# Performance work log

Measured on AMD Instinct MI355X. Metric: run time of the kernel, lower is better.

Reference implementation:

```python
import jax, jax.numpy as jnp
import numpy as np

B, N, NP, K, C_IN, C, H = 16, 4096, 1024, 32, 128, 256, 4
C_G = C_IN + 3  # grouped feature dim (use_xyz concat of relative coords)
EPS = 1e-3      # keras LayerNormalization default epsilon


def setup_inputs() -> dict:
    key = jax.random.key(0)
    ks = jax.random.split(key, 16)
    s = 0.05
    return {
        "xyz": jax.random.normal(ks[0], (B, N, 3), jnp.float32),
        "newxyz": jax.random.normal(ks[1], (B, NP, 3), jnp.float32),
        "feature_input": jax.random.normal(ks[2], (B, N, C_IN), jnp.float32),
        "w_qkv": jax.random.normal(ks[3], (C_G, 3 * C), jnp.float32) * s,
        "proj_w": jax.random.normal(ks[4], (C, C), jnp.float32) * s,
        "proj_b": jnp.zeros((C,), jnp.float32),
        "dense_w": jax.random.normal(ks[5], (C_G, C), jnp.float32) * s,
        "dense_b": jnp.zeros((C,), jnp.float32),
        "fc1_w": jax.random.normal(ks[6], (C, 2 * C), jnp.float32) * s,
        "fc1_b": jnp.zeros((2 * C,), jnp.float32),
        "fc2_w": jax.random.normal(ks[7], (2 * C, C), jnp.float32) * s,
        "fc2_b": jnp.zeros((C,), jnp.float32),
        "n1_g": jnp.ones((C_G,), jnp.float32),
        "n1_b": jnp.zeros((C_G,), jnp.float32),
        "n2_g": jnp.ones((C,), jnp.float32),
        "n2_b": jnp.zeros((C,), jnp.float32),
        "group_num": K,
        "training": True,
    }


def _layernorm(x, g, b):
    m = jnp.mean(x, axis=-1, keepdims=True)
    v = jnp.mean(jnp.square(x - m), axis=-1, keepdims=True)
    return (x - m) * jax.lax.rsqrt(v + EPS) * g + b


def _sample_and_group(newxyz, group_num, xyz, feats):
    # squared pairwise distances (B, NP, N)
    d2 = (jnp.sum(newxyz**2, -1)[:, :, None]
          - 2.0 * jnp.einsum('bpc,bnc->bpn', newxyz, xyz)
          + jnp.sum(xyz**2, -1)[:, None, :])
    _, idx = jax.lax.top_k(-d2, group_num)            # (B, NP, K) nearest
    b_idx = jnp.arange(newxyz.shape[0])[:, None, None]
    grouped_xyz = xyz[b_idx, idx] - newxyz[:, :, None, :]   # (B, NP, K, 3)
    grouped_feat = feats[b_idx, idx]                        # (B, NP, K, C_IN)
    return jnp.concatenate([grouped_xyz, grouped_feat], axis=-1)


def _self_attention(x, w_qkv, proj_w, proj_b):
    b, n, k = x.shape[0], x.shape[1], x.shape[2]
    d = C // H
    qkv = jnp.einsum('bnkc,cd->bnkd', x, w_qkv)
    qkv = qkv.reshape(b, n, k, 3, H, d)
    qkv = jnp.transpose(qkv, (3, 0, 1, 4, 2, 5))      # (3, B, NP, H, K, d)
    q, kk, v = qkv[0], qkv[1], qkv[2]
    qm = jnp.max(q, axis=-2, keepdims=True)           # (B, NP, H, 1, d)
    attn = jnp.einsum('bnhqd,bnhkd->bnhqk', qm, kk) * (C ** -0.5)
    attn = jax.nn.softmax(attn, axis=-1)
    out = jnp.einsum('bnhqk,bnhkd->bnhqd', attn, v)[..., 0, :]  # (B, NP, H, d)
    out = out.reshape(b, n, C)
    return jax.nn.relu(out @ proj_w + proj_b)


def reference(xyz, newxyz, feature_input, w_qkv, proj_w, proj_b, dense_w,
              dense_b, fc1_w, fc1_b, fc2_w, fc2_b, n1_g, n1_b, n2_g, n2_b,
              group_num, training):
    gf = _sample_and_group(newxyz, group_num, xyz, feature_input)  # (B,NP,K,C_G)
    feat = _self_attention(_layernorm(gf, n1_g, n1_b), w_qkv, proj_w, proj_b)
    feat = feat + jax.nn.relu(jnp.max(gf, axis=-2) @ dense_w + dense_b)
    f2 = _layernorm(feat, n2_g, n2_b)
    f2 = jax.nn.relu(f2 @ fc1_w + fc1_b)
    f2 = f2 @ fc2_w + fc2_b
    return f2 + feat
```

## Files before the change

kernel.cpp:

```cpp
#include <hip/hip_runtime.h>
#include <hip/hip_bf16.h>

typedef __hip_bfloat16 bf16;

#define Bn   16
#define Nn   4096
#define NPn  1024
#define Kn   32
#define CINn 128
#define CGn  131
#define Cn   256
#define Hn   4
#define KPAD 160
#define XBS  168
#define XFS2 136
#define GFS  136

typedef __attribute__((ext_vector_type(8))) short frag_ab;
typedef __attribute__((ext_vector_type(4))) float frag_cd;

__device__ __forceinline__ float b2f(bf16 x) { return __bfloat162float(x); }
__device__ __forceinline__ bf16  f2b(float x) { return __float2bfloat16(x); }
__device__ __forceinline__ short f2bs(float x) {
  union { bf16 h; short s; } u; u.h = __float2bfloat16(x); return u.s;
}
__device__ __forceinline__ float bs2f(short s) {
  union { short v; bf16 h; } u; u.v = s; return __bfloat162float(u.h);
}
__device__ __forceinline__ unsigned f2ord(float f) {
  unsigned u = __float_as_uint(f);
  return u ^ ((u >> 31) ? 0xffffffffu : 0x80000000u);
}

__global__ __launch_bounds__(256) void xyzw_prep_kernel(
    const float* __restrict__ xyz, float4* __restrict__ xyzw) {
  const int i = blockIdx.x * 256 + threadIdx.x;
  const float x = xyz[i*3 + 0];
  const float y = xyz[i*3 + 1];
  const float z = xyz[i*3 + 2];
  const float sx = __fadd_rn(__fadd_rn(__fmul_rn(x,x), __fmul_rn(y,y)),
                             __fmul_rn(z,z));
  xyzw[i] = make_float4(x, y, z, sx);
}

__global__ __launch_bounds__(256) void knn_kernel(const float4* __restrict__ xyzw,
                                                  const float* __restrict__ newxyz,
                                                  int* __restrict__ idx_out) {
  constexpr int CAP = 2048;
  __shared__ unsigned long long tmin[256];
  __shared__ __align__(16) unsigned long long cand[CAP + 4];
  __shared__ unsigned long long wtau[4];
  __shared__ unsigned long long wred[4];
  __shared__ int scnt;
  const int bp  = blockIdx.x;
  const int b   = bp >> 10;
  const int tid = threadIdx.x;
  const float qx = newxyz[bp*3 + 0];
  const float qy = newxyz[bp*3 + 1];
  const float qz = newxyz[bp*3 + 2];
  const float sn = __fadd_rn(__fadd_rn(__fmul_rn(qx,qx), __fmul_rn(qy,qy)),
                             __fmul_rn(qz,qz));
  const float4* xb = xyzw + (size_t)b * Nn;
  unsigned long long key[16];
  unsigned long long lmin = ~0ull;
  #pragma unroll
  for (int s = 0; s < 16; ++s) {
    const int n = s*256 + tid;
    const float4 xw = xb[n];
    const float dot = __fadd_rn(__fadd_rn(__fmul_rn(qx,xw.x), __fmul_rn(qy,xw.y)),
                                __fmul_rn(qz,xw.z));
    const float d2 = __fadd_rn(__fsub_rn(sn, __fmul_rn(2.0f, dot)), xw.w);
    key[s] = ((unsigned long long)f2ord(d2) << 32) | (unsigned)n;
    if (key[s] < lmin) lmin = key[s];
  }
  const int lane = tid & 63, wv = tid >> 6;

  if (tid == 0) scnt = 0;
  tmin[tid] = lmin;
  __syncthreads();

  {
    const unsigned long long* wt = &tmin[wv * 64];
    int rk = 0;
    #pragma unroll 8
    for (int j = 0; j < 64; ++j) rk += (wt[j] < lmin) ? 1 : 0;
    if (rk == 15) wtau[wv] = lmin;
  }
  __syncthreads();
  unsigned long long tau = wtau[0];
  if (wtau[1] < tau) tau = wtau[1];
  if (wtau[2] < tau) tau = wtau[2];
  if (wtau[3] < tau) tau = wtau[3];

  #pragma unroll
  for (int s = 0; s < 16; ++s) {
    if (key[s] <= tau) {
      const int p = atomicAdd(&scnt, 1);
      if (p < CAP) cand[p] = key[s];
    }
  }
  __syncthreads();
  const int m = scnt;

  if (m >= Kn && m <= CAP) {
    if (tid < 4) cand[m + tid] = ~0ull;
    __syncthreads();
    const int m4 = (m + 3) & ~3;
    for (int t = tid; t < m; t += 256) {
      const unsigned long long mykey = cand[t];
      int r = 0;
      for (int j = 0; j < m4; j += 4) {
        r += (cand[j+0] < mykey) ? 1 : 0;
        r += (cand[j+1] < mykey) ? 1 : 0;
        r += (cand[j+2] < mykey) ? 1 : 0;
        r += (cand[j+3] < mykey) ? 1 : 0;
      }
      if (r < Kn) idx_out[(size_t)bp*Kn + r] = (int)(mykey & 0xffffffffu);
    }
  } else {
    for (int s = 0; s < Kn; ++s) {
      unsigned long long mm = lmin;
      #pragma unroll
      for (int d = 32; d; d >>= 1) {
        const unsigned lo = __shfl_xor((unsigned)(mm & 0xffffffffu), d, 64);
        const unsigned hi = __shfl_xor((unsigned)(mm >> 32), d, 64);
        const unsigned long long o = ((unsigned long long)hi << 32) | lo;
        if (o < mm) mm = o;
      }
      if (lane == 0) wred[wv] = mm;
      __syncthreads();
      unsigned long long best = wred[0];
      if (wred[1] < best) best = wred[1];
      if (wred[2] < best) best = wred[2];
      if (wred[3] < best) best = wred[3];
      __syncthreads();
      const int n = (int)(best & 0xffffffffu);
      if (tid == 0) idx_out[(size_t)bp*Kn + s] = n;
      if ((n & 255) == tid) {
        const int slot = n >> 8;
        #pragma unroll
        for (int t = 0; t < 16; ++t) if (t == slot) key[t] = ~0ull;
        unsigned long long m2 = ~0ull;
        #pragma unroll
        for (int t = 0; t < 16; ++t) if (key[t] < m2) m2 = key[t];
        lmin = m2;
      }
    }
  }
}

__global__ __launch_bounds__(256) void wprep_all_kernel(
    const float* __restrict__ w_qkv, const float* __restrict__ proj_w,
    const float* __restrict__ dense_w, const float* __restrict__ fc1_w,
    const float* __restrict__ fc2_w, short* __restrict__ o_qkv,
    short* __restrict__ o_proj, short* __restrict__ o_dense,
    short* __restrict__ o_fc1, short* __restrict__ o_fc2) {
  const int blk = blockIdx.x;
  const float* W; short* out; int K, N, nnt, remap, base;
  if      (blk <  480) { W=w_qkv;   out=o_qkv;   K=CGn; N=768; nnt=48; remap=1; base=0;    }
  else if (blk <  736) { W=proj_w;  out=o_proj;  K=Cn;  N=256; nnt=16; remap=0; base=480;  }
  else if (blk <  896) { W=dense_w; out=o_dense; K=CGn; N=256; nnt=16; remap=1; base=736;  }
  else if (blk < 1408) { W=fc1_w;   out=o_fc1;   K=Cn;  N=512; nnt=32; remap=0; base=896;  }
  else                 { W=fc2_w;   out=o_fc2;   K=512; N=256; nnt=16; remap=0; base=1408; }
  const int t = (blk - base) * 256 + threadIdx.x;
  const int j    = t & 7;
  const int lane = (t >> 3) & 63;
  const int nt   = (t >> 9) % nnt;
  const int kt   = (t >> 9) / nnt;
  const int k = kt*32 + (lane >> 4)*8 + j;
  const int n = nt*16 + (lane & 15);
  int krow = k;
  if (remap) krow = (k < 128) ? k + 3 : k - 128;
  out[t] = (k < K) ? f2bs(W[(size_t)krow*N + n]) : (short)0;
}

__global__ __launch_bounds__(256, 3) void fused_attn_kernel(
    const float* __restrict__ xyz, const float* __restrict__ newxyz,
    const float* __restrict__ featin, const short* __restrict__ wfrag,
    const float* __restrict__ n1g, const float* __restrict__ n1b,
    const int* __restrict__ idx, bf16* __restrict__ attnout,
    bf16* __restrict__ gfmax) {
  __shared__ __align__(16) short Xs[64 * XBS];
  __shared__ float sg[CGn], sb[CGn];
  __shared__ int sidx[64];
  const int bp0 = blockIdx.x * 2;
  const int b   = bp0 >> 10;
  const int tid = threadIdx.x;
  if (tid < 64) {
    int n = idx[(size_t)bp0*Kn + tid];
    sidx[tid] = ((unsigned)n < (unsigned)Nn) ? n : 0;
  }
  if (tid < CGn) {
    const int rj = (tid < 128) ? tid + 3 : tid - 128;
    sg[tid] = n1g[rj];
    sb[tid] = n1b[rj];
  }
  __syncthreads();
  const int kk = tid >> 3, sub = tid & 7;
  float4 r[2][4];
  float ex[2] = {0.f, 0.f};
  #pragma unroll
  for (int p = 0; p < 2; ++p) {
    const int row = p*32 + kk;
    const float* frow = featin + ((size_t)b*Nn + sidx[row])*CINn;
    #pragma unroll
    for (int i = 0; i < 4; ++i) r[p][i] = *(const float4*)(frow + sub*4 + 32*i);
    if (sub < 3)
      ex[p] = xyz[((size_t)b*Nn + sidx[row])*3 + sub] - newxyz[(bp0+p)*3 + sub];
  }
  #pragma unroll
  for (int p = 0; p < 2; ++p) {
    const int row = p*32 + kk;
    #pragma unroll
    for (int i = 0; i < 4; ++i) {
      short4 s4 = { f2bs(r[p][i].x), f2bs(r[p][i].y), f2bs(r[p][i].z), f2bs(r[p][i].w) };
      *(short4*)&Xs[row*XFS2 + sub*4 + 32*i] = s4;
    }
    if (sub < 3) Xs[row*XFS2 + 128 + sub] = f2bs(ex[p]);
  }
  float mean[2], rstd[2];
  #pragma unroll
  for (int p = 0; p < 2; ++p) {
    float s = ex[p], s2 = ex[p]*ex[p];
    #pragma unroll
    for (int i = 0; i < 4; ++i) {
      s  += r[p][i].x + r[p][i].y + r[p][i].z + r[p][i].w;
      s2 += r[p][i].x*r[p][i].x + r[p][i].y*r[p][i].y
          + r[p][i].z*r[p][i].z + r[p][i].w*r[p][i].w;
    }
    s  += __shfl_xor(s, 1, 64);  s  += __shfl_xor(s, 2, 64);  s  += __shfl_xor(s, 4, 64);
    s2 += __shfl_xor(s2, 1, 64); s2 += __shfl_xor(s2, 2, 64); s2 += __shfl_xor(s2, 4, 64);
    mean[p] = s * (1.0f/CGn);
    const float var = s2 * (1.0f/CGn) - mean[p]*mean[p];
    rstd[p] = rsqrtf(var + 1e-3f);
  }
  __syncthreads();
  #pragma unroll
  for (int p = 0; p < 2; ++p) {
    if (tid < GFS) {
      float m = 0.f;
      if (tid < CGn) {
        m = -1e30f;
        #pragma unroll
        for (int k2 = 0; k2 < Kn; ++k2)
          m = fmaxf(m, bs2f(Xs[(p*32 + k2)*XFS2 + tid]));
      }
      gfmax[(size_t)(bp0+p)*GFS + tid] = f2b(m);
    }
  }
  __syncthreads();
  #pragma unroll
  for (int p = 0; p < 2; ++p) {
    const int row = p*32 + kk;
    #pragma unroll
    for (int i = 0; i < 4; ++i) {
      const float4 g4 = *(const float4*)&sg[sub*4 + 32*i];
      const float4 b4 = *(const float4*)&sb[sub*4 + 32*i];
      short4 s4;
      s4.x = f2bs((r[p][i].x - mean[p])*rstd[p]*g4.x + b4.x);
      s4.y = f2bs((r[p][i].y - mean[p])*rstd[p]*g4.y + b4.y);
      s4.z = f2bs((r[p][i].z - mean[p])*rstd[p]*g4.z + b4.z);
      s4.w = f2bs((r[p][i].w - mean[p])*rstd[p]*g4.w + b4.w);
      *(short4*)&Xs[row*XBS + sub*4 + 32*i] = s4;
    }
    if (sub < 3)
      Xs[row*XBS + 128 + sub] = f2bs((ex[p] - mean[p])*rstd[p]*sg[128+sub] + sb[128+sub]);
  }
  #pragma unroll
  for (int u = 0; u < 8; ++u) {
    const int e = u*256 + tid;
    const int row = e >> 5, jj = 131 + (e & 31);
    if (jj < 160) Xs[row*XBS + jj] = 0;
  }
  __syncthreads();
  const int lane = tid & 63, w = tid >> 6;
  const int col = lane & 15, quad = lane >> 4;
  float qm[2][4], aw[2][2][4], inv[2];
  {
    #pragma unroll 1
    for (int half = 0; half < 2; ++half) {
      frag_cd acc[2][4] = {};
      __builtin_amdgcn_s_setprio(1);
      for (int kt = 0; kt < 5; ++kt) {
        const int ko = kt*32 + quad*8;
        frag_ab a[4];
        #pragma unroll
        for (int mt = 0; mt < 4; ++mt)
          a[mt] = *(const frag_ab*)&Xs[(mt*16 + col)*XBS + ko];
        #pragma unroll
        for (int ntl = 0; ntl < 2; ++ntl) {
          const int nt = w*4 + half*2 + ntl;
          const frag_ab bfr = *(const frag_ab*)(wfrag + ((size_t)(kt*48 + nt)*64 + lane)*8);
          #pragma unroll
          for (int mt = 0; mt < 4; ++mt)
            acc[ntl][mt] = __builtin_amdgcn_mfma_f32_16x16x32_bf16(a[mt], bfr, acc[ntl][mt], 0, 0, 0);
        }
      }
      __builtin_amdgcn_s_setprio(0);
      #pragma unroll
      for (int p = 0; p < 2; ++p)
        #pragma unroll
        for (int ntl = 0; ntl < 2; ++ntl) {
          float m = -1e30f;
          #pragma unroll
          for (int mtl = 0; mtl < 2; ++mtl)
            #pragma unroll
            for (int rr = 0; rr < 4; ++rr) m = fmaxf(m, acc[ntl][p*2+mtl][rr]);
          m = fmaxf(m, __shfl_xor(m, 16, 64));
          m = fmaxf(m, __shfl_xor(m, 32, 64));
          qm[p][half*2 + ntl] = m;
        }
    }
  }
  {
    float pp[2][2][4] = {};
    #pragma unroll 1
    for (int half = 0; half < 2; ++half) {
      frag_cd acc[2][4] = {};
      __builtin_amdgcn_s_setprio(1);
      for (int kt = 0; kt < 5; ++kt) {
        const int ko = kt*32 + quad*8;
        frag_ab a[4];
        #pragma unroll
        for (int mt = 0; mt < 4; ++mt)
          a[mt] = *(const frag_ab*)&Xs[(mt*16 + col)*XBS + ko];
        #pragma unroll
        for (int ntl = 0; ntl < 2; ++ntl) {
          const int nt = 16 + w*4 + half*2 + ntl;
          const frag_ab bfr = *(const frag_ab*)(wfrag + ((size_t)(kt*48 + nt)*64 + lane)*8);
          #pragma unroll
          for (int mt = 0; mt < 4; ++mt)
            acc[ntl][mt] = __builtin_amdgcn_mfma_f32_16x16x32_bf16(a[mt], bfr, acc[ntl][mt], 0, 0, 0);
        }
      }
      __builtin_amdgcn_s_setprio(0);
      #pragma unroll
      for (int p = 0; p < 2; ++p)
        #pragma unroll
        for (int mtl = 0; mtl < 2; ++mtl)
          #pragma unroll
          for (int rr = 0; rr < 4; ++rr) {
            #pragma unroll
            for (int ntl = 0; ntl < 2; ++ntl)
              pp[p][mtl][rr] = fmaf(qm[p][half*2 + ntl], acc[ntl][p*2+mtl][rr], pp[p][mtl][rr]);
          }
    }
    #pragma unroll
    for (int p = 0; p < 2; ++p) {
      float lg[2][4];
      #pragma unroll
      for (int mtl = 0; mtl < 2; ++mtl)
        #pragma unroll
        for (int rr = 0; rr < 4; ++rr) {
          float v = pp[p][mtl][rr];
          #pragma unroll
          for (int d = 1; d < 16; d <<= 1) v += __shfl_xor(v, d, 64);
          lg[mtl][rr] = v * 0.0625f;
        }
      float mx = -1e30f;
      #pragma unroll
      for (int mtl = 0; mtl < 2; ++mtl)
        #pragma unroll
        for (int rr = 0; rr < 4; ++rr) mx = fmaxf(mx, lg[mtl][rr]);
      mx = fmaxf(mx, __shfl_xor(mx, 16, 64));
      mx = fmaxf(mx, __shfl_xor(mx, 32, 64));
      float ssum = 0.f;
      #pragma unroll
      for (int mtl = 0; mtl < 2; ++mtl)
        #pragma unroll
        for (int rr = 0; rr < 4; ++rr) { aw[p][mtl][rr] = expf(lg[mtl][rr] - mx); ssum += aw[p][mtl][rr]; }
      ssum += __shfl_xor(ssum, 16, 64);
      ssum += __shfl_xor(ssum, 32, 64);
      inv[p] = 1.f / ssum;
    }
  }
  {
    #pragma unroll 1
    for (int half = 0; half < 2; ++half) {
      frag_cd acc[2][4] = {};
      __builtin_amdgcn_s_setprio(1);
      for (int kt = 0; kt < 5; ++kt) {
        const int ko = kt*32 + quad*8;
        frag_ab a[4];
        #pragma unroll
        for (int mt = 0; mt < 4; ++mt)
          a[mt] = *(const frag_ab*)&Xs[(mt*16 + col)*XBS + ko];
        #pragma unroll
        for (int ntl = 0; ntl < 2; ++ntl) {
          const int nt = 32 + w*4 + half*2 + ntl;
          const frag_ab bfr = *(const frag_ab*)(wfrag + ((size_t)(kt*48 + nt)*64 + lane)*8);
          #pragma unroll
          for (int mt = 0; mt < 4; ++mt)
            acc[ntl][mt] = __builtin_amdgcn_mfma_f32_16x16x32_bf16(a[mt], bfr, acc[ntl][mt], 0, 0, 0);
        }
      }
      __builtin_amdgcn_s_setprio(0);
      #pragma unroll
      for (int p = 0; p < 2; ++p)
        #pragma unroll
        for (int ntl = 0; ntl < 2; ++ntl) {
          float o = 0.f;
          #pragma unroll
          for (int mtl = 0; mtl < 2; ++mtl)
            #pragma unroll
            for (int rr = 0; rr < 4; ++rr) o = fmaf(aw[p][mtl][rr], acc[ntl][p*2+mtl][rr], o);
          o += __shfl_xor(o, 16, 64);
          o += __shfl_xor(o, 32, 64);
          if (quad == 0)
            attnout[(size_t)(bp0+p)*Cn + w*64 + (half*2 + ntl)*16 + col] = f2b(o * inv[p]);
        }
    }
  }
}

template<bool RELU, bool ADD_S, bool OUT_BF16>
__global__ __launch_bounds__(256) void mfma_gemm_kernel(
    const bf16* __restrict__ A, int lda, int Ka,
    const short* __restrict__ Wf, int nnt_total, int N,
    const float* __restrict__ bias, const bf16* __restrict__ S,
    void* __restrict__ Dv) {
  __shared__ __align__(16) short As[64*40];
  const int m0 = blockIdx.y * 64;
  const int n0 = blockIdx.x * 128;
  const int tid = threadIdx.x, lane = tid & 63, w = tid >> 6;
  const int col = lane & 15, quad = lane >> 4;
  const int row = tid >> 2, c8 = (tid & 3) * 8;
  frag_cd acc[4][2] = {};
  const int nkt = (Ka + 31) >> 5;
  for (int kt = 0; kt < nkt; ++kt) {
    const int k0 = kt*32 + c8;
    frag_ab av = {0,0,0,0,0,0,0,0};
    if (k0 + 8 <= Ka)
      av = *(const frag_ab*)((const short*)A + (size_t)(m0+row)*lda + k0);
    __syncthreads();
    *(frag_ab*)&As[row*40 + c8] = av;
    __syncthreads();
    frag_ab afr[4];
    #pragma unroll
    for (int mt = 0; mt < 4; ++mt)
      afr[mt] = *(const frag_ab*)&As[(mt*16 + col)*40 + quad*8];
    #pragma unroll
    for (int ntl = 0; ntl < 2; ++ntl) {
      const int nt = (n0 >> 4) + w*2 + ntl;
      const frag_ab bfr = *(const frag_ab*)(Wf + ((size_t)(kt*nnt_total + nt)*64 + lane)*8);
      #pragma unroll
      for (int mt = 0; mt < 4; ++mt)
        acc[mt][ntl] = __builtin_amdgcn_mfma_f32_16x16x32_bf16(afr[mt], bfr, acc[mt][ntl], 0, 0, 0);
    }
  }
  #pragma unroll
  for (int ntl = 0; ntl < 2; ++ntl) {
    const int n = n0 + w*32 + ntl*16 + col;
    const float bv = bias[n];
    #pragma unroll
    for (int mt = 0; mt < 4; ++mt) {
      #pragma unroll
      for (int r = 0; r < 4; ++r) {
        const int m = m0 + mt*16 + quad*4 + r;
        float v = acc[mt][ntl][r] + bv;
        if (RELU) v = fmaxf(v, 0.f);
        if (ADD_S) v += b2f(S[(size_t)m*N + n]);
        if (OUT_BF16) ((bf16*)Dv)[(size_t)m*N + n] = f2b(v);
        else          ((float*)Dv)[(size_t)m*N + n] = v;
      }
    }
  }
}

__global__ __launch_bounds__(256) void dual_gemm_kernel(
    const bf16* __restrict__ A1, const short* __restrict__ W1,
    const bf16* __restrict__ A2, const short* __restrict__ W2,
    const float* __restrict__ b1, const float* __restrict__ b2,
    bf16* __restrict__ D) {
  __shared__ __align__(16) short As[64*40];
  const int m0 = blockIdx.y * 64;
  const int n0 = blockIdx.x * 128;
  const int tid = threadIdx.x, lane = tid & 63, w = tid >> 6;
  const int col = lane & 15, quad = lane >> 4;
  const int row = tid >> 2, c8 = (tid & 3) * 8;
  frag_cd acc1[4][2] = {}, acc2[4][2] = {};
  for (int kt = 0; kt < 8; ++kt) {
    const frag_ab av = *(const frag_ab*)((const short*)A1 + (size_t)(m0+row)*Cn + kt*32 + c8);
    __syncthreads();
    *(frag_ab*)&As[row*40 + c8] = av;
    __syncthreads();
    frag_ab afr[4];
    #pragma unroll
    for (int mt = 0; mt < 4; ++mt)
      afr[mt] = *(const frag_ab*)&As[(mt*16 + col)*40 + quad*8];
    #pragma unroll
    for (int ntl = 0; ntl < 2; ++ntl) {
      const int nt = (n0 >> 4) + w*2 + ntl;
      const frag_ab bfr = *(const frag_ab*)(W1 + ((size_t)(kt*16 + nt)*64 + lane)*8);
      #pragma unroll
      for (int mt = 0; mt < 4; ++mt)
        acc1[mt][ntl] = __builtin_amdgcn_mfma_f32_16x16x32_bf16(afr[mt], bfr, acc1[mt][ntl], 0, 0, 0);
    }
  }
  for (int kt = 0; kt < 5; ++kt) {
    const int k0 = kt*32 + c8;
    frag_ab av = {0,0,0,0,0,0,0,0};
    if (k0 + 8 <= GFS)
      av = *(const frag_ab*)((const short*)A2 + (size_t)(m0+row)*GFS + k0);
    __syncthreads();
    *(frag_ab*)&As[row*40 + c8] = av;
    __syncthreads();
    frag_ab afr[4];
    #pragma unroll
    for (int mt = 0; mt < 4; ++mt)
      afr[mt] = *(const frag_ab*)&As[(mt*16 + col)*40 + quad*8];
    #pragma unroll
    for (int ntl = 0; ntl < 2; ++ntl) {
      const int nt = (n0 >> 4) + w*2 + ntl;
      const frag_ab bfr = *(const frag_ab*)(W2 + ((size_t)(kt*16 + nt)*64 + lane)*8);
      #pragma unroll
      for (int mt = 0; mt < 4; ++mt)
        acc2[mt][ntl] = __builtin_amdgcn_mfma_f32_16x16x32_bf16(afr[mt], bfr, acc2[mt][ntl], 0, 0, 0);
    }
  }
  #pragma unroll
  for (int ntl = 0; ntl < 2; ++ntl) {
    const int n = n0 + w*32 + ntl*16 + col;
    const float bv1 = b1[n], bv2 = b2[n];
    #pragma unroll
    for (int mt = 0; mt < 4; ++mt) {
      #pragma unroll
      for (int r = 0; r < 4; ++r) {
        const int m = m0 + mt*16 + quad*4 + r;
        const float v = fmaxf(acc1[mt][ntl][r] + bv1, 0.f)
                      + fmaxf(acc2[mt][ntl][r] + bv2, 0.f);
        D[(size_t)m*Cn + n] = f2b(v);
      }
    }
  }
}

__global__ __launch_bounds__(256) void ln2_kernel(const bf16* __restrict__ feat,
                                                  const float* __restrict__ g,
                                                  const float* __restrict__ b,
                                                  bf16* __restrict__ out) {
  const int r = blockIdx.x*4 + (threadIdx.x >> 6), lane = threadIdx.x & 63;
  float vv[4];
  #pragma unroll
  for (int c = 0; c < 4; ++c) vv[c] = b2f(feat[(size_t)r*Cn + lane*4 + c]);
  float s  = vv[0] + vv[1] + vv[2] + vv[3];
  float s2 = vv[0]*vv[0] + vv[1]*vv[1] + vv[2]*vv[2] + vv[3]*vv[3];
  #pragma unroll
  for (int d = 32; d; d >>= 1) { s += __shfl_xor(s, d, 64); s2 += __shfl_xor(s2, d, 64); }
  const float mean = s * (1.f/256.f);
  const float var  = s2 * (1.f/256.f) - mean*mean;
  const float rstd = rsqrtf(var + 1e-3f);
  #pragma unroll
  for (int c = 0; c < 4; ++c) {
    const int cc = lane*4 + c;
    out[(size_t)r*Cn + cc] = f2b((vv[c] - mean)*rstd*g[cc] + b[cc]);
  }
}

extern "C" void kernel_launch(void* const* d_in, const int* in_sizes, int n_in,
                              void* d_out, int out_size, void* d_ws, size_t ws_size,
                              hipStream_t stream) {
  const float* xyz     = (const float*)d_in[0];
  const float* newxyz  = (const float*)d_in[1];
  const float* featin  = (const float*)d_in[2];
  const float* w_qkv   = (const float*)d_in[3];
  const float* proj_w  = (const float*)d_in[4];
  const float* proj_b  = (const float*)d_in[5];
  const float* dense_w = (const float*)d_in[6];
  const float* dense_b = (const float*)d_in[7];
  const float* fc1_w   = (const float*)d_in[8];
  const float* fc1_b   = (const float*)d_in[9];
  const float* fc2_w   = (const float*)d_in[10];
  const float* fc2_b   = (const float*)d_in[11];
  const float* n1g     = (const float*)d_in[12];
  const float* n1b     = (const float*)d_in[13];
  const float* n2g     = (const float*)d_in[14];
  const float* n2b     = (const float*)d_in[15];

  char*  ws     = (char*)d_ws;
  short* wqkv   = (short*)(ws + 0);
  short* wproj  = (short*)(ws + 245760);
  short* wdense = (short*)(ws + 376832);
  short* wfc1   = (short*)(ws + 458752);
  short* wfc2   = (short*)(ws + 720896);
  bf16*  featB  = (bf16*)(ws + 1048576);
  bf16*  attnA  = (bf16*)(ws + 9437184);
  bf16*  gfmax  = (bf16*)(ws + 17825792);
  int*   idxws  = (int*) (ws + 22282240);
  bf16*  fc1out = (bf16*)(ws + 24379392);
  float4* xyzw  = (float4*)(ws + 24379392);

  const int M = Bn * NPn;

  xyzw_prep_kernel<<<dim3(Bn*Nn/256), dim3(256), 0, stream>>>(xyz, xyzw);
  knn_kernel<<<dim3(M), dim3(256), 0, stream>>>(xyzw, newxyz, idxws);
  wprep_all_kernel<<<dim3(1920), dim3(256), 0, stream>>>(
      w_qkv, proj_w, dense_w, fc1_w, fc2_w, wqkv, wproj, wdense, wfc1, wfc2);

  fused_attn_kernel<<<dim3(M/2), dim3(256), 0, stream>>>(
      xyz, newxyz, featin, wqkv, n1g, n1b, idxws, attnA, gfmax);
  dual_gemm_kernel<<<dim3(2, M/64), dim3(256), 0, stream>>>(
      attnA, wproj, gfmax, wdense, proj_b, dense_b, featB);
  ln2_kernel<<<dim3(M/4), dim3(256), 0, stream>>>(featB, n2g, n2b, attnA);
  mfma_gemm_kernel<true, false, true><<<dim3(4, M/64), dim3(256), 0, stream>>>(
      attnA, Cn, Cn, wfc1, 32, 512, fc1_b, (const bf16*)nullptr, fc1out);
  mfma_gemm_kernel<false, true, false><<<dim3(2, M/64), dim3(256), 0, stream>>>(
      fc1out, 512, 512, wfc2, 16, Cn, fc2_b, featB, d_out);
}
```

Measured before the change: 420.2 us.

## Fuse LayerNorm2 into dual GEMM epilogue and drop MFMA priority hints

```diff
diff --git a/kernel.cpp b/kernel.cpp
--- a/kernel.cpp
+++ b/kernel.cpp
@@ -280,7 +280,6 @@
     #pragma unroll 1
     for (int half = 0; half < 2; ++half) {
       frag_cd acc[2][4] = {};
-      __builtin_amdgcn_s_setprio(1);
       for (int kt = 0; kt < 5; ++kt) {
         const int ko = kt*32 + quad*8;
         frag_ab a[4];
@@ -296,7 +295,6 @@
             acc[ntl][mt] = __builtin_amdgcn_mfma_f32_16x16x32_bf16(a[mt], bfr, acc[ntl][mt], 0, 0, 0);
         }
       }
-      __builtin_amdgcn_s_setprio(0);
       #pragma unroll
       for (int p = 0; p < 2; ++p)
         #pragma unroll
@@ -317,7 +315,6 @@
     #pragma unroll 1
     for (int half = 0; half < 2; ++half) {
       frag_cd acc[2][4] = {};
-      __builtin_amdgcn_s_setprio(1);
       for (int kt = 0; kt < 5; ++kt) {
         const int ko = kt*32 + quad*8;
         frag_ab a[4];
@@ -333,7 +330,6 @@
             acc[ntl][mt] = __builtin_amdgcn_mfma_f32_16x16x32_bf16(a[mt], bfr, acc[ntl][mt], 0, 0, 0);
         }
       }
-      __builtin_amdgcn_s_setprio(0);
       #pragma unroll
       for (int p = 0; p < 2; ++p)
         #pragma unroll
@@ -378,7 +374,6 @@
     #pragma unroll 1
     for (int half = 0; half < 2; ++half) {
       frag_cd acc[2][4] = {};
-      __builtin_amdgcn_s_setprio(1);
       for (int kt = 0; kt < 5; ++kt) {
         const int ko = kt*32 + quad*8;
         frag_ab a[4];
@@ -394,7 +389,6 @@
             acc[ntl][mt] = __builtin_amdgcn_mfma_f32_16x16x32_bf16(a[mt], bfr, acc[ntl][mt], 0, 0, 0);
         }
       }
-      __builtin_amdgcn_s_setprio(0);
       #pragma unroll
       for (int p = 0; p < 2; ++p)
         #pragma unroll
@@ -467,18 +461,19 @@
   }
 }
 
-__global__ __launch_bounds__(256) void dual_gemm_kernel(
-    const bf16* __restrict__ A1, const short* __restrict__ W1,
+__global__ void dual_gemm_ln2_kernel(
+    const bf16* A1, const short* __restrict__ W1,
     const bf16* __restrict__ A2, const short* __restrict__ W2,
     const float* __restrict__ b1, const float* __restrict__ b2,
-    bf16* __restrict__ D) {
+    const float* __restrict__ g2, const float* __restrict__ bb2,
+    bf16* __restrict__ featB, bf16* ln2out) {
   __shared__ __align__(16) short As[64*40];
-  const int m0 = blockIdx.y * 64;
-  const int n0 = blockIdx.x * 128;
+  __shared__ __align__(16) short Fs[64*256];
+  const int m0 = blockIdx.x * 64;
   const int tid = threadIdx.x, lane = tid & 63, w = tid >> 6;
   const int col = lane & 15, quad = lane >> 4;
   const int row = tid >> 2, c8 = (tid & 3) * 8;
-  frag_cd acc1[4][2] = {}, acc2[4][2] = {};
+  frag_cd acc1[4][4] = {}, acc2[4][4] = {};
   for (int kt = 0; kt < 8; ++kt) {
     const frag_ab av = *(const frag_ab*)((const short*)A1 + (size_t)(m0+row)*Cn + kt*32 + c8);
     __syncthreads();
@@ -489,8 +484,8 @@
     for (int mt = 0; mt < 4; ++mt)
       afr[mt] = *(const frag_ab*)&As[(mt*16 + col)*40 + quad*8];
     #pragma unroll
-    for (int ntl = 0; ntl < 2; ++ntl) {
-      const int nt = (n0 >> 4) + w*2 + ntl;
+    for (int ntl = 0; ntl < 4; ++ntl) {
+      const int nt = w*4 + ntl;
       const frag_ab bfr = *(const frag_ab*)(W1 + ((size_t)(kt*16 + nt)*64 + lane)*8);
       #pragma unroll
       for (int mt = 0; mt < 4; ++mt)
@@ -510,8 +505,8 @@
     for (int mt = 0; mt < 4; ++mt)
       afr[mt] = *(const frag_ab*)&As[(mt*16 + col)*40 + quad*8];
     #pragma unroll
-    for (int ntl = 0; ntl < 2; ++ntl) {
-      const int nt = (n0 >> 4) + w*2 + ntl;
+    for (int ntl = 0; ntl < 4; ++ntl) {
+      const int nt = w*4 + ntl;
       const frag_ab bfr = *(const frag_ab*)(W2 + ((size_t)(kt*16 + nt)*64 + lane)*8);
       #pragma unroll
       for (int mt = 0; mt < 4; ++mt)
@@ -519,41 +514,51 @@
     }
   }
   #pragma unroll
-  for (int ntl = 0; ntl < 2; ++ntl) {
-    const int n = n0 + w*32 + ntl*16 + col;
+  for (int ntl = 0; ntl < 4; ++ntl) {
+    const int n = w*64 + ntl*16 + col;
     const float bv1 = b1[n], bv2 = b2[n];
     #pragma unroll
     for (int mt = 0; mt < 4; ++mt) {
       #pragma unroll
       for (int r = 0; r < 4; ++r) {
-        const int m = m0 + mt*16 + quad*4 + r;
+        const int m = mt*16 + quad*4 + r;
         const float v = fmaxf(acc1[mt][ntl][r] + bv1, 0.f)
                       + fmaxf(acc2[mt][ntl][r] + bv2, 0.f);
-        D[(size_t)m*Cn + n] = f2b(v);
-      }
-    }
-  }
-}
-
-__global__ __launch_bounds__(256) void ln2_kernel(const bf16* __restrict__ feat,
-                                                  const float* __restrict__ g,
-                                                  const float* __restrict__ b,
-                                                  bf16* __restrict__ out) {
-  const int r = blockIdx.x*4 + (threadIdx.x >> 6), lane = threadIdx.x & 63;
-  float vv[4];
-  #pragma unroll
-  for (int c = 0; c < 4; ++c) vv[c] = b2f(feat[(size_t)r*Cn + lane*4 + c]);
-  float s  = vv[0] + vv[1] + vv[2] + vv[3];
-  float s2 = vv[0]*vv[0] + vv[1]*vv[1] + vv[2]*vv[2] + vv[3]*vv[3];
-  #pragma unroll
-  for (int d = 32; d; d >>= 1) { s += __shfl_xor(s, d, 64); s2 += __shfl_xor(s2, d, 64); }
-  const float mean = s * (1.f/256.f);
-  const float var  = s2 * (1.f/256.f) - mean*mean;
-  const float rstd = rsqrtf(var + 1e-3f);
-  #pragma unroll
-  for (int c = 0; c < 4; ++c) {
-    const int cc = lane*4 + c;
-    out[(size_t)r*Cn + cc] = f2b((vv[c] - mean)*rstd*g[cc] + b[cc]);
+        const short sv = f2bs(v);
+        Fs[m*256 + n] = sv;
+        featB[(size_t)(m0+m)*Cn + n] = f2b(bs2f(sv));
+      }
+    }
+  }
+  __syncthreads();
+  {
+    const int r2 = tid >> 2, seg = (tid & 3) * 64;
+    float s = 0.f, s2 = 0.f;
+    #pragma unroll
+    for (int i = 0; i < 16; ++i) {
+      const short4 q = *(const short4*)&Fs[r2*256 + seg + i*4];
+      const float v0 = bs2f(q.x), v1 = bs2f(q.y), v2 = bs2f(q.z), v3 = bs2f(q.w);
+      s  += v0 + v1 + v2 + v3;
+      s2 += v0*v0 + v1*v1 + v2*v2 + v3*v3;
+    }
+    s  += __shfl_xor(s, 1, 64);  s  += __shfl_xor(s, 2, 64);
+    s2 += __shfl_xor(s2, 1, 64); s2 += __shfl_xor(s2, 2, 64);
+    const float mean = s * (1.f/256.f);
+    const float var  = s2 * (1.f/256.f) - mean*mean;
+    const float rstd = rsqrtf(var + 1e-3f);
+    #pragma unroll
+    for (int i = 0; i < 16; ++i) {
+      const int cc = seg + i*4;
+      const short4 q = *(const short4*)&Fs[r2*256 + cc];
+      const float4 gg = *(const float4*)&g2[cc];
+      const float4 bb = *(const float4*)&bb2[cc];
+      short4 o;
+      o.x = f2bs((bs2f(q.x) - mean)*rstd*gg.x + bb.x);
+      o.y = f2bs((bs2f(q.y) - mean)*rstd*gg.y + bb.y);
+      o.z = f2bs((bs2f(q.z) - mean)*rstd*gg.z + bb.z);
+      o.w = f2bs((bs2f(q.w) - mean)*rstd*gg.w + bb.w);
+      *(short4*)((short*)ln2out + (size_t)(m0+r2)*Cn + cc) = o;
+    }
   }
 }
 
@@ -599,9 +604,8 @@
 
   fused_attn_kernel<<<dim3(M/2), dim3(256), 0, stream>>>(
       xyz, newxyz, featin, wqkv, n1g, n1b, idxws, attnA, gfmax);
-  dual_gemm_kernel<<<dim3(2, M/64), dim3(256), 0, stream>>>(
-      attnA, wproj, gfmax, wdense, proj_b, dense_b, featB);
-  ln2_kernel<<<dim3(M/4), dim3(256), 0, stream>>>(featB, n2g, n2b, attnA);
+  dual_gemm_ln2_kernel<<<dim3(M/64), dim3(256), 0, stream>>>(
+      attnA, wproj, gfmax, wdense, proj_b, dense_b, n2g, n2b, featB, attnA);
   mfma_gemm_kernel<true, false, true><<<dim3(4, M/64), dim3(256), 0, stream>>>(
       attnA, Cn, Cn, wfc1, 32, 512, fc1_b, (const bf16*)nullptr, fc1out);
   mfma_gemm_kernel<false, true, false><<<dim3(2, M/64), dim3(256), 0, stream>>>(
```

New measurement: 433.6 us. 3.2% more time.
